# Optimization experiments

Hardware: AMD Instinct MI355X
Metric: run time of the kernel (lower is better)

## Reference

```python
import jax, jax.numpy as jnp
import numpy as np

N, E = 50000, 800000
IN, H, D = 64, 4, 16          # in_feats, num_heads, head_size (IN == H*D -> identity skip)
NT, ET = 2, 2                 # num node / edge types


def setup_inputs() -> dict:
    key = jax.random.key(0)
    ks = jax.random.split(key, 13)
    s = 0.05
    return {
        "x": jax.random.normal(ks[0], (N, IN), jnp.float32),
        # TypedLinear weights: one [in,out] matrix per node type (DGL TypedLinear, no bias)
        "Wk": jax.random.normal(ks[1], (NT, IN, H * D), jnp.float32) * s,
        "Wq": jax.random.normal(ks[2], (NT, IN, H * D), jnp.float32) * s,
        "Wv": jax.random.normal(ks[3], (NT, IN, H * D), jnp.float32) * s,
        "Wa": jax.random.normal(ks[4], (NT, H * D, H * D), jnp.float32) * s,
        # per-head, per-edge-type relation matrices (relation_att / relation_msg)
        "Ratt": jax.random.normal(ks[5], (H, ET, D, D), jnp.float32) * s,
        "Rmsg": jax.random.normal(ks[6], (H, ET, D, D), jnp.float32) * s,
        "pri": jnp.ones((H, ET), jnp.float32),   # relation_pri
        "skip": jnp.ones((NT,), jnp.float32),    # skip gate per node type
        "ntype": jax.random.randint(ks[7], (N,), 0, NT),
        "etype": jax.random.randint(ks[8], (E,), 0, ET),
        "src": jax.random.randint(ks[9], (E,), 0, N),
        "dst": jax.random.randint(ks[10], (E,), 0, N),
    }


def _typed_linear(x, W, types):
    # x:[N,I], W:[T,I,O], types:[N] -> y[n] = x[n] @ W[types[n]]
    # T is tiny (2): compute all types densely, then select per node.
    y_all = jnp.einsum('ni,tio->tno', x, W)
    return y_all[types, jnp.arange(x.shape[0])]


def reference(x, Wk, Wq, Wv, Wa, Ratt, Rmsg, pri, skip, ntype, etype, src, dst):
    n = x.shape[0]
    k = _typed_linear(x, Wk, ntype).reshape(n, H, D)
    q = _typed_linear(x, Wq, ntype).reshape(n, H, D)
    v = _typed_linear(x, Wv, ntype).reshape(n, H, D)
    # relation transforms per edge type, computed once at node level (ET is tiny),
    # then gathered per edge: equivalent to per-edge TypedLinear in DGL's message fn.
    katt = jnp.einsum('nhd,htdf->thnf', k, Ratt)   # [ET,H,N,D]
    vmsg = jnp.einsum('nhd,htdf->thnf', v, Rmsg)   # [ET,H,N,D]
    kw = katt[etype, :, src]                       # [E,H,D]
    m = vmsg[etype, :, src]                        # [E,H,D]
    qd = q[dst]                                    # [E,H,D]
    # attention logits: (K W_att) . Q * relation_pri / sqrt(d)
    a = (kw * qd).sum(-1) * pri[:, etype].T / jnp.sqrt(jnp.float32(D))  # [E,H]
    # edge softmax over incoming edges of each destination node (stable)
    amax = jax.ops.segment_max(a, dst, num_segments=n)                  # [N,H]
    ae = jnp.exp(a - amax[dst])
    asum = jax.ops.segment_sum(ae, dst, num_segments=n)
    attn = ae / asum[dst]                                               # [E,H]
    # scatter-aggregate messages
    h = jax.ops.segment_sum(m * attn[:, :, None], dst, num_segments=n)  # [N,H,D]
    # target-specific output projection (dropout is identity in eval)
    h = _typed_linear(h.reshape(n, H * D), Wa, ntype)                   # [N,H*D]
    # sigmoid-gated skip (in_feats == H*D so identity residual)
    alpha = jax.nn.sigmoid(skip)[ntype][:, None]
    return h * alpha + x * (1.0 - alpha)
```

## Files before the change

kernel.cpp:

```cpp
#include <hip/hip_runtime.h>
#include <math.h>
#include <stdint.h>

#define N_NODES 50000
#define N_EDGES 800000
#define NT_TYPES 2
#define ET_TYPES 2
#define NB_SCAN ((N_NODES + 255) / 256)
#define M_COLS 320
#define M_PER_T (64 * M_COLS)
#define PROJ_GRID ((N_NODES + 63) / 64)
#define SCAT_GRID ((N_EDGES + 255) / 256)
#define AGG_GRID (N_NODES / 16)
#define MAXDEG 64
#define LOG2E 1.44269504088896f
#define HSTRIDE 36

typedef __attribute__((ext_vector_type(8))) short short8v;
typedef __attribute__((ext_vector_type(4))) float float4v;

__device__ __forceinline__ unsigned int f32_to_bf16(float f) {
  unsigned int u = __float_as_uint(f);
  return (u + 0x7FFFu + ((u >> 16) & 1u)) >> 16;
}

__device__ __forceinline__ float row16_sum(float p) {
  int r;
  r = __builtin_amdgcn_update_dpp(0, __float_as_int(p), 0x128, 0xf, 0xf, false);
  p += __int_as_float(r);
  r = __builtin_amdgcn_update_dpp(0, __float_as_int(p), 0x124, 0xf, 0xf, false);
  p += __int_as_float(r);
  r = __builtin_amdgcn_update_dpp(0, __float_as_int(p), 0x122, 0xf, 0xf, false);
  p += __int_as_float(r);
  r = __builtin_amdgcn_update_dpp(0, __float_as_int(p), 0x121, 0xf, 0xf, false);
  p += __int_as_float(r);
  return p;
}

__global__ void prep_kernel(
    const float* __restrict__ Wk, const float* __restrict__ Wq,
    const float* __restrict__ Wv, const float* __restrict__ Wa,
    const float* __restrict__ Ratt, const float* __restrict__ Rmsg,
    const float* __restrict__ pri,
    unsigned short* __restrict__ M2b, unsigned short* __restrict__ Wa2b,
    int* __restrict__ deg) {
  const int idx = blockIdx.x * 256 + threadIdx.x;
  if (idx < N_NODES) deg[idx] = 0;
  if (idx < NT_TYPES * 4096) {
    int t = idx >> 12;
    int rem = idx & 4095;
    int col = rem >> 6, k = rem & 63;
    Wa2b[idx] = (unsigned short)f32_to_bf16(Wa[(size_t)t * 4096 + k * 64 + col]);
  }
  if (idx < NT_TYPES * M_PER_T) {
    int t = idx / M_PER_T;
    int rem = idx % M_PER_T;
    int col = rem / 64;
    int k = rem % 64;
    float val;
    if (col < 64) {
      val = Wq[(size_t)t * 4096 + k * 64 + col];
    } else {
      int cc = col - 64;
      int et = cc >> 7;
      int r = cc & 127;
      int c = r >> 1;
      int half = r & 1;
      int h = c >> 4, f = c & 15;
      const float* W = half ? Wv : Wk;
      const float* R = half ? Rmsg : Ratt;
      float s = 0.f;
#pragma unroll
      for (int d = 0; d < 16; ++d)
        s = fmaf(W[(size_t)t * 4096 + k * 64 + h * 16 + d],
                 R[(((size_t)h * ET_TYPES + et) * 16 + d) * 16 + f], s);
      if (half == 0) s *= pri[h * ET_TYPES + et] * 0.25f * LOG2E;
      val = s;
    }
    M2b[idx] = (unsigned short)f32_to_bf16(val);
  }
}

__global__ __launch_bounds__(256) void projscatter_kernel(
    const float* __restrict__ x,
    const unsigned short* __restrict__ M2b,
    const int* __restrict__ ntype,
    unsigned short* __restrict__ qb, unsigned int* __restrict__ kvb,
    const int* __restrict__ src, const int* __restrict__ dst,
    const int* __restrict__ etype, int* __restrict__ deg,
    int* __restrict__ csr) {
  const int bid = blockIdx.x;
  if (bid >= PROJ_GRID) {
    const int e = (bid - PROJ_GRID) * 256 + threadIdx.x;
    if (e < N_EDGES) {
      int d = dst[e];
      int r = atomicAdd(&deg[d], 1);
      __builtin_nontemporal_store((etype[e] * N_NODES + src[e]) << 6,
                                  &csr[(d << 6) + r]);
    }
    return;
  }
  const int wave = threadIdx.x >> 6;
  const int lane = threadIdx.x & 63;
  const int base = bid * 64 + wave * 16;
  const int l15 = lane & 15;
  const int lq = lane >> 4;

  const int nidA = min(base + l15, N_NODES - 1);
  const float4* xr = reinterpret_cast<const float4*>(x + (size_t)nidA * 64);
  const float4 xa0 = xr[lq * 2 + 0];
  const float4 xa1 = xr[lq * 2 + 1];
  const float4 xb0 = xr[8 + lq * 2 + 0];
  const float4 xb1 = xr[8 + lq * 2 + 1];
  union { short8v v; unsigned int u[4]; } A0u, A1u;
  A0u.u[0] = f32_to_bf16(xa0.x) | (f32_to_bf16(xa0.y) << 16);
  A0u.u[1] = f32_to_bf16(xa0.z) | (f32_to_bf16(xa0.w) << 16);
  A0u.u[2] = f32_to_bf16(xa1.x) | (f32_to_bf16(xa1.y) << 16);
  A0u.u[3] = f32_to_bf16(xa1.z) | (f32_to_bf16(xa1.w) << 16);
  A1u.u[0] = f32_to_bf16(xb0.x) | (f32_to_bf16(xb0.y) << 16);
  A1u.u[1] = f32_to_bf16(xb0.z) | (f32_to_bf16(xb0.w) << 16);
  A1u.u[2] = f32_to_bf16(xb1.x) | (f32_to_bf16(xb1.y) << 16);
  A1u.u[3] = f32_to_bf16(xb1.z) | (f32_to_bf16(xb1.w) << 16);
  const short8v A0 = A0u.v;
  const short8v A1 = A1u.v;

  const int n0 = min(base + lq * 4 + 0, N_NODES - 1);
  const int n1 = min(base + lq * 4 + 1, N_NODES - 1);
  const int n2 = min(base + lq * 4 + 2, N_NODES - 1);
  const int n3 = min(base + lq * 4 + 3, N_NODES - 1);
  const int t0 = ntype[n0], t1 = ntype[n1], t2 = ntype[n2], t3 = ntype[n3];

#pragma unroll
  for (int ct = 0; ct < 20; ++ct) {
    const int colb = ct * 16 + l15;
    const size_t boff = (size_t)colb * 64 + lq * 8;
    const short8v B00 = *reinterpret_cast<const short8v*>(M2b + boff);
    const short8v B01 = *reinterpret_cast<const short8v*>(M2b + boff + 32);
    const short8v B10 = *reinterpret_cast<const short8v*>(M2b + M_PER_T + boff);
    const short8v B11 = *reinterpret_cast<const short8v*>(M2b + M_PER_T + boff + 32);
    float4v C0 = {0.f, 0.f, 0.f, 0.f};
    C0 = __builtin_amdgcn_mfma_f32_16x16x32_bf16(A0, B00, C0, 0, 0, 0);
    C0 = __builtin_amdgcn_mfma_f32_16x16x32_bf16(A1, B01, C0, 0, 0, 0);
    float4v C1 = {0.f, 0.f, 0.f, 0.f};
    C1 = __builtin_amdgcn_mfma_f32_16x16x32_bf16(A0, B10, C1, 0, 0, 0);
    C1 = __builtin_amdgcn_mfma_f32_16x16x32_bf16(A1, B11, C1, 0, 0, 0);

    const float v0 = t0 ? C1[0] : C0[0];
    const float v1 = t1 ? C1[1] : C0[1];
    const float v2 = t2 ? C1[2] : C0[2];
    const float v3 = t3 ? C1[3] : C0[3];

    if (ct < 4) {
      qb[(size_t)n0 * 64 + colb] = (unsigned short)f32_to_bf16(v0);
      qb[(size_t)n1 * 64 + colb] = (unsigned short)f32_to_bf16(v1);
      qb[(size_t)n2 * 64 + colb] = (unsigned short)f32_to_bf16(v2);
      qb[(size_t)n3 * 64 + colb] = (unsigned short)f32_to_bf16(v3);
    } else {
      const float p0 = __shfl_xor(v0, 1, 64);
      const float p1 = __shfl_xor(v1, 1, 64);
      const float p2 = __shfl_xor(v2, 1, 64);
      const float p3 = __shfl_xor(v3, 1, 64);
      if ((lane & 1) == 0) {
        const int cc = colb - 64;
        const int et = cc >> 7;
        const int c = (cc & 127) >> 1;
        const size_t b0 = ((size_t)et * N_NODES) * 64 + c;
        kvb[b0 + (size_t)n0 * 64] = f32_to_bf16(v0) | (f32_to_bf16(p0) << 16);
        kvb[b0 + (size_t)n1 * 64] = f32_to_bf16(v1) | (f32_to_bf16(p1) << 16);
        kvb[b0 + (size_t)n2 * 64] = f32_to_bf16(v2) | (f32_to_bf16(p2) << 16);
        kvb[b0 + (size_t)n3 * 64] = f32_to_bf16(v3) | (f32_to_bf16(p3) << 16);
      }
    }
  }
}

__device__ __forceinline__ void edge_update(unsigned int wrd, float qd,
                                            float& srun, float& acc) {
  float kw = __uint_as_float(wrd << 16);
  float mv = __uint_as_float(wrd & 0xFFFF0000u);
  float w = __builtin_amdgcn_exp2f(row16_sum(kw * qd));
  srun += w;
  acc = fmaf(mv, w, acc);
}

__global__ __launch_bounds__(256) void agg_out_kernel(
    const unsigned short* __restrict__ qb, const unsigned int* __restrict__ kvb,
    const int* __restrict__ deg, const int* __restrict__ csr,
    const unsigned short* __restrict__ Wa2b, const float* __restrict__ x,
    const float* __restrict__ skip, const int* __restrict__ ntype,
    float* __restrict__ out) {
  __shared__ unsigned int hlds[16 * HSTRIDE];
  const int wave = threadIdx.x >> 6;
  const int lane = threadIdx.x & 63;
  const int base = blockIdx.x * 16;

  for (int half = 0; half < 2; ++half) {
    const int lrowA = wave * 4 + half * 2;
    const int nA = __builtin_amdgcn_readfirstlane(base + lrowA);
    const int nB = __builtin_amdgcn_readfirstlane(base + lrowA + 1);
    const float qdA = __uint_as_float((unsigned int)qb[(size_t)nA * 64 + lane] << 16);
    const float qdB = __uint_as_float((unsigned int)qb[(size_t)nB * 64 + lane] << 16);
    const int eA = __builtin_amdgcn_readfirstlane(deg[nA]);
    const int eB = __builtin_amdgcn_readfirstlane(deg[nB]);
    const int* cA = csr + (nA << 6);
    const int* cB = csr + (nB << 6);

    float sA = 0.f, aA = 0.f, sB = 0.f, aB = 0.f;
    const int m = min(eA, eB);
    int j = 0;
    for (; j + 4 <= m; j += 4) {
      int pA0 = __builtin_amdgcn_readfirstlane(cA[j + 0]);
      int pA1 = __builtin_amdgcn_readfirstlane(cA[j + 1]);
      int pA2 = __builtin_amdgcn_readfirstlane(cA[j + 2]);
      int pA3 = __builtin_amdgcn_readfirstlane(cA[j + 3]);
      int pB0 = __builtin_amdgcn_readfirstlane(cB[j + 0]);
      int pB1 = __builtin_amdgcn_readfirstlane(cB[j + 1]);
      int pB2 = __builtin_amdgcn_readfirstlane(cB[j + 2]);
      int pB3 = __builtin_amdgcn_readfirstlane(cB[j + 3]);
      unsigned int wA0 = kvb[(unsigned)pA0 + lane];
      unsigned int wA1 = kvb[(unsigned)pA1 + lane];
      unsigned int wA2 = kvb[(unsigned)pA2 + lane];
      unsigned int wA3 = kvb[(unsigned)pA3 + lane];
      unsigned int wB0 = kvb[(unsigned)pB0 + lane];
      unsigned int wB1 = kvb[(unsigned)pB1 + lane];
      unsigned int wB2 = kvb[(unsigned)pB2 + lane];
      unsigned int wB3 = kvb[(unsigned)pB3 + lane];
      edge_update(wA0, qdA, sA, aA);
      edge_update(wB0, qdB, sB, aB);
      edge_update(wA1, qdA, sA, aA);
      edge_update(wB1, qdB, sB, aB);
      edge_update(wA2, qdA, sA, aA);
      edge_update(wB2, qdB, sB, aB);
      edge_update(wA3, qdA, sA, aA);
      edge_update(wB3, qdB, sB, aB);
    }
    int jA = j;
    for (; jA + 4 <= eA; jA += 4) {
      int p0 = __builtin_amdgcn_readfirstlane(cA[jA + 0]);
      int p1 = __builtin_amdgcn_readfirstlane(cA[jA + 1]);
      int p2 = __builtin_amdgcn_readfirstlane(cA[jA + 2]);
      int p3 = __builtin_amdgcn_readfirstlane(cA[jA + 3]);
      unsigned int w0 = kvb[(unsigned)p0 + lane];
      unsigned int w1 = kvb[(unsigned)p1 + lane];
      unsigned int w2 = kvb[(unsigned)p2 + lane];
      unsigned int w3 = kvb[(unsigned)p3 + lane];
      edge_update(w0, qdA, sA, aA);
      edge_update(w1, qdA, sA, aA);
      edge_update(w2, qdA, sA, aA);
      edge_update(w3, qdA, sA, aA);
    }
    for (; jA < eA; ++jA) {
      int p = __builtin_amdgcn_readfirstlane(cA[jA]);
      edge_update(kvb[(unsigned)p + lane], qdA, sA, aA);
    }
    int jB = j;
    for (; jB + 4 <= eB; jB += 4) {
      int p0 = __builtin_amdgcn_readfirstlane(cB[jB + 0]);
      int p1 = __builtin_amdgcn_readfirstlane(cB[jB + 1]);
      int p2 = __builtin_amdgcn_readfirstlane(cB[jB + 2]);
      int p3 = __builtin_amdgcn_readfirstlane(cB[jB + 3]);
      unsigned int w0 = kvb[(unsigned)p0 + lane];
      unsigned int w1 = kvb[(unsigned)p1 + lane];
      unsigned int w2 = kvb[(unsigned)p2 + lane];
      unsigned int w3 = kvb[(unsigned)p3 + lane];
      edge_update(w0, qdB, sB, aB);
      edge_update(w1, qdB, sB, aB);
      edge_update(w2, qdB, sB, aB);
      edge_update(w3, qdB, sB, aB);
    }
    for (; jB < eB; ++jB) {
      int p = __builtin_amdgcn_readfirstlane(cB[jB]);
      edge_update(kvb[(unsigned)p + lane], qdB, sB, aB);
    }

    float hvA = (sA > 0.f) ? (aA / sA) : 0.f;
    float hvB = (sB > 0.f) ? (aB / sB) : 0.f;
    float prA = __shfl_xor(hvA, 1, 64);
    float prB = __shfl_xor(hvB, 1, 64);
    if ((lane & 1) == 0) {
      hlds[lrowA * HSTRIDE + (lane >> 1)] =
          f32_to_bf16(hvA) | (f32_to_bf16(prA) << 16);
      hlds[(lrowA + 1) * HSTRIDE + (lane >> 1)] =
          f32_to_bf16(hvB) | (f32_to_bf16(prB) << 16);
    }
  }
  __syncthreads();

  const int l15 = lane & 15;
  const int lq = lane >> 4;
  const short8v A0 = *reinterpret_cast<const short8v*>(&hlds[l15 * HSTRIDE + lq * 4]);
  const short8v A1 = *reinterpret_cast<const short8v*>(&hlds[l15 * HSTRIDE + 16 + lq * 4]);

  const int n0 = base + lq * 4 + 0;
  const int n1 = base + lq * 4 + 1;
  const int n2 = base + lq * 4 + 2;
  const int n3 = base + lq * 4 + 3;
  const int t0 = ntype[n0], t1 = ntype[n1], t2 = ntype[n2], t3 = ntype[n3];

  const float alpha0 = 1.f / (1.f + __expf(-skip[0]));
  const float alpha1 = 1.f / (1.f + __expf(-skip[1]));

  const int colb = wave * 16 + l15;
  const size_t boff = (size_t)colb * 64 + lq * 8;
  const short8v B00 = *reinterpret_cast<const short8v*>(Wa2b + boff);
  const short8v B01 = *reinterpret_cast<const short8v*>(Wa2b + boff + 32);
  const short8v B10 = *reinterpret_cast<const short8v*>(Wa2b + 4096 + boff);
  const short8v B11 = *reinterpret_cast<const short8v*>(Wa2b + 4096 + boff + 32);
  float4v C0 = {0.f, 0.f, 0.f, 0.f};
  C0 = __builtin_amdgcn_mfma_f32_16x16x32_bf16(A0, B00, C0, 0, 0, 0);
  C0 = __builtin_amdgcn_mfma_f32_16x16x32_bf16(A1, B01, C0, 0, 0, 0);
  float4v C1 = {0.f, 0.f, 0.f, 0.f};
  C1 = __builtin_amdgcn_mfma_f32_16x16x32_bf16(A0, B10, C1, 0, 0, 0);
  C1 = __builtin_amdgcn_mfma_f32_16x16x32_bf16(A1, B11, C1, 0, 0, 0);

  const float al0 = t0 ? alpha1 : alpha0;
  const float al1 = t1 ? alpha1 : alpha0;
  const float al2 = t2 ? alpha1 : alpha0;
  const float al3 = t3 ? alpha1 : alpha0;
  const float v0 = t0 ? C1[0] : C0[0];
  const float v1 = t1 ? C1[1] : C0[1];
  const float v2 = t2 ? C1[2] : C0[2];
  const float v3 = t3 ? C1[3] : C0[3];

  const size_t o0 = (size_t)n0 * 64 + colb;
  const size_t o1 = (size_t)n1 * 64 + colb;
  const size_t o2 = (size_t)n2 * 64 + colb;
  const size_t o3 = (size_t)n3 * 64 + colb;
  out[o0] = v0 * al0 + x[o0] * (1.f - al0);
  out[o1] = v1 * al1 + x[o1] * (1.f - al1);
  out[o2] = v2 * al2 + x[o2] * (1.f - al2);
  out[o3] = v3 * al3 + x[o3] * (1.f - al3);
}

extern "C" void kernel_launch(void* const* d_in, const int* in_sizes, int n_in,
                              void* d_out, int out_size, void* d_ws, size_t ws_size,
                              hipStream_t stream) {
  const float* x    = (const float*)d_in[0];
  const float* Wk   = (const float*)d_in[1];
  const float* Wq   = (const float*)d_in[2];
  const float* Wv   = (const float*)d_in[3];
  const float* Wa   = (const float*)d_in[4];
  const float* Ratt = (const float*)d_in[5];
  const float* Rmsg = (const float*)d_in[6];
  const float* pri  = (const float*)d_in[7];
  const float* skip = (const float*)d_in[8];
  const int* ntype  = (const int*)d_in[9];
  const int* etype  = (const int*)d_in[10];
  const int* src    = (const int*)d_in[11];
  const int* dst    = (const int*)d_in[12];
  float* out = (float*)d_out;

  unsigned short* qb = (unsigned short*)d_ws;
  unsigned int* kvb = (unsigned int*)(qb + (size_t)N_NODES * 64);
  int* deg = (int*)(kvb + (size_t)ET_TYPES * N_NODES * 64);
  int* csr = deg + N_NODES;
  unsigned short* M2b = (unsigned short*)
      (((uintptr_t)(csr + (size_t)N_NODES * MAXDEG) + 255) & ~(uintptr_t)255);
  unsigned short* Wa2b = (unsigned short*)
      (((uintptr_t)(M2b + NT_TYPES * M_PER_T) + 255) & ~(uintptr_t)255);

  prep_kernel<<<NB_SCAN, 256, 0, stream>>>(
      Wk, Wq, Wv, Wa, Ratt, Rmsg, pri, M2b, Wa2b, deg);

  projscatter_kernel<<<PROJ_GRID + SCAT_GRID, 256, 0, stream>>>(
      x, M2b, ntype, qb, kvb, src, dst, etype, deg, csr);

  agg_out_kernel<<<AGG_GRID, 256, 0, stream>>>(
      qb, (const unsigned int*)kvb, deg, csr, Wa2b, x, skip, ntype, out);
}
```

Before: 102.0 us.

## Split CSR build into sharded count, prefix, and fill passes

Replaces the single-pass atomic CSR scatter with a two-pass build. Degrees are first counted into 8 sharded counters keyed by block index, then a per-node prefix over the shards gives each shard a base offset, and a fill pass places edges using atomics on the shard counters. The aim is to cut same-address atomic contention on the degree array. The cost is two extra kernel launches, a second read of the dst array, and a larger counter buffer to zero.

```diff
diff --git a/kernel.cpp b/kernel.cpp
--- a/kernel.cpp
+++ b/kernel.cpp
@@ -6,12 +6,13 @@
 #define N_EDGES 800000
 #define NT_TYPES 2
 #define ET_TYPES 2
-#define NB_SCAN ((N_NODES + 255) / 256)
 #define M_COLS 320
 #define M_PER_T (64 * M_COLS)
 #define PROJ_GRID ((N_NODES + 63) / 64)
-#define SCAT_GRID ((N_EDGES + 255) / 256)
+#define EDGE_GRID ((N_EDGES + 255) / 256)
 #define AGG_GRID (N_NODES / 16)
+#define PREP_GRID ((8 * N_NODES + 255) / 256)
+#define NB_SCAN ((N_NODES + 255) / 256)
 #define MAXDEG 64
 #define LOG2E 1.44269504088896f
 #define HSTRIDE 36
@@ -43,9 +44,9 @@
     const float* __restrict__ Ratt, const float* __restrict__ Rmsg,
     const float* __restrict__ pri,
     unsigned short* __restrict__ M2b, unsigned short* __restrict__ Wa2b,
-    int* __restrict__ deg) {
+    int* __restrict__ cnt8) {
   const int idx = blockIdx.x * 256 + threadIdx.x;
-  if (idx < N_NODES) deg[idx] = 0;
+  if (idx < 8 * N_NODES) cnt8[idx] = 0;
   if (idx < NT_TYPES * 4096) {
     int t = idx >> 12;
     int rem = idx & 4095;
@@ -81,23 +82,18 @@
   }
 }
 
-__global__ __launch_bounds__(256) void projscatter_kernel(
+__global__ __launch_bounds__(256) void countproj_kernel(
     const float* __restrict__ x,
     const unsigned short* __restrict__ M2b,
-    const int* __restrict__ ntype,
+    const int* __restrict__ ntype, const int* __restrict__ dst,
     unsigned short* __restrict__ qb, unsigned int* __restrict__ kvb,
-    const int* __restrict__ src, const int* __restrict__ dst,
-    const int* __restrict__ etype, int* __restrict__ deg,
-    int* __restrict__ csr) {
+    int* __restrict__ cnt8) {
   const int bid = blockIdx.x;
   if (bid >= PROJ_GRID) {
-    const int e = (bid - PROJ_GRID) * 256 + threadIdx.x;
-    if (e < N_EDGES) {
-      int d = dst[e];
-      int r = atomicAdd(&deg[d], 1);
-      __builtin_nontemporal_store((etype[e] * N_NODES + src[e]) << 6,
-                                  &csr[(d << 6) + r]);
-    }
+    const int cb = bid - PROJ_GRID;
+    const int e = cb * 256 + threadIdx.x;
+    if (e < N_EDGES)
+      atomicAdd(&cnt8[(cb & 7) * N_NODES + dst[e]], 1);
     return;
   }
   const int wave = threadIdx.x >> 6;
@@ -171,6 +167,32 @@
         kvb[b0 + (size_t)n3 * 64] = f32_to_bf16(v3) | (f32_to_bf16(p3) << 16);
       }
     }
+  }
+}
+
+__global__ void prefix_kernel(int* __restrict__ cnt8, int* __restrict__ deg) {
+  const int n = blockIdx.x * 256 + threadIdx.x;
+  if (n >= N_NODES) return;
+  int run = 0;
+#pragma unroll
+  for (int r = 0; r < 8; ++r) {
+    int c = cnt8[r * N_NODES + n];
+    cnt8[r * N_NODES + n] = run;
+    run += c;
+  }
+  deg[n] = run;
+}
+
+__global__ void fill_kernel(const int* __restrict__ src,
+                            const int* __restrict__ dst,
+                            const int* __restrict__ etype,
+                            int* __restrict__ cnt8, int* __restrict__ csr) {
+  const int e = blockIdx.x * 256 + threadIdx.x;
+  if (e < N_EDGES) {
+    int d = dst[e];
+    int slot = atomicAdd(&cnt8[(blockIdx.x & 7) * N_NODES + d], 1);
+    __builtin_nontemporal_store((etype[e] * N_NODES + src[e]) << 6,
+                                &csr[(d << 6) + slot]);
   }
 }
 
@@ -352,18 +374,23 @@
 
   unsigned short* qb = (unsigned short*)d_ws;
   unsigned int* kvb = (unsigned int*)(qb + (size_t)N_NODES * 64);
-  int* deg = (int*)(kvb + (size_t)ET_TYPES * N_NODES * 64);
-  int* csr = deg + N_NODES;
+  int* deg  = (int*)(kvb + (size_t)ET_TYPES * N_NODES * 64);
+  int* cnt8 = deg + N_NODES;
+  int* csr  = cnt8 + 8 * N_NODES;
   unsigned short* M2b = (unsigned short*)
       (((uintptr_t)(csr + (size_t)N_NODES * MAXDEG) + 255) & ~(uintptr_t)255);
   unsigned short* Wa2b = (unsigned short*)
       (((uintptr_t)(M2b + NT_TYPES * M_PER_T) + 255) & ~(uintptr_t)255);
 
-  prep_kernel<<<NB_SCAN, 256, 0, stream>>>(
-      Wk, Wq, Wv, Wa, Ratt, Rmsg, pri, M2b, Wa2b, deg);
-
-  projscatter_kernel<<<PROJ_GRID + SCAT_GRID, 256, 0, stream>>>(
-      x, M2b, ntype, qb, kvb, src, dst, etype, deg, csr);
+  prep_kernel<<<PREP_GRID, 256, 0, stream>>>(
+      Wk, Wq, Wv, Wa, Ratt, Rmsg, pri, M2b, Wa2b, cnt8);
+
+  countproj_kernel<<<PROJ_GRID + EDGE_GRID, 256, 0, stream>>>(
+      x, M2b, ntype, dst, qb, kvb, cnt8);
+
+  prefix_kernel<<<NB_SCAN, 256, 0, stream>>>(cnt8, deg);
+
+  fill_kernel<<<EDGE_GRID, 256, 0, stream>>>(src, dst, etype, cnt8, csr);
 
   agg_out_kernel<<<AGG_GRID, 256, 0, stream>>>(
       qb, (const unsigned int*)kvb, deg, csr, Wa2b, x, skip, ntype, out);
```

Measured after the change: 162.8 us. 59.6% more time.
